# Performance work log

Hardware: AMD Instinct MI355X
Metric: run time of the kernel (lower is better)

The kernel has to match this reference:

```python
import jax, jax.numpy as jnp
import numpy as np

D_MODEL = 512
D_HEAD = 64
N_HEADS = D_MODEL // D_HEAD  # 8
KSIZE = 7


def setup_inputs() -> dict:
    key = jax.random.key(0)
    k1, k2, k3 = jax.random.split(key, 3)
    x = jax.random.normal(k1, (2, 48, 48, D_MODEL), dtype=jnp.float32)
    # torch Linear(d, 3d, bias=False): y = x @ W.T ; store transposed weight directly
    w_qkv = jax.random.normal(k2, (D_MODEL, 3 * D_MODEL), dtype=jnp.float32) * 0.02
    w_out = jax.random.normal(k3, (D_MODEL, D_MODEL), dtype=jnp.float32) * 0.02
    return {"x": x, "w_qkv": w_qkv, "w_out": w_out}


def _nbhd_idx(L, k):
    # NATTEN semantics: window centered at each pixel, shifted (clamped) to stay
    # fully inside the image near borders. Returns [L, k] absolute indices.
    start = jnp.clip(jnp.arange(L) - k // 2, 0, L - k)
    return start[:, None] + jnp.arange(k)[None, :]


def reference(x, w_qkv, w_out):
    n, h, w, _ = x.shape
    qkv = (x @ w_qkv).reshape(n, h, w, 3, N_HEADS, D_HEAD)
    qkv = jnp.transpose(qkv, (3, 0, 4, 1, 2, 5))  # [3, n, nh, h, w, e]
    q, k, v = qkv[0], qkv[1], qkv[2]
    q = q / jnp.asarray(D_HEAD, q.dtype) ** 0.5

    ih = _nbhd_idx(h, KSIZE)  # [h, k]
    iw = _nbhd_idx(w, KSIZE)  # [w, k]
    IH = ih[:, None, :, None]  # [h,1,k,1]
    IW = iw[None, :, None, :]  # [1,w,1,k]

    # gather per-pixel 2D neighborhoods: [n, nh, h, w, ka, kb, e]
    k_nb = k[:, :, IH, IW, :]
    logits = jnp.einsum('nghwe,nghwabe->nghwab', q, k_nb)
    logits = logits.reshape(n, N_HEADS, h, w, KSIZE * KSIZE)
    attn = jax.nn.softmax(logits, axis=-1).reshape(n, N_HEADS, h, w, KSIZE, KSIZE)

    v_nb = v[:, :, IH, IW, :]
    o = jnp.einsum('nghwab,nghwabe->nghwe', attn, v_nb)  # [n, nh, h, w, e]
    o = jnp.transpose(o, (0, 2, 3, 1, 4)).reshape(n, h, w, N_HEADS * D_HEAD)
    return o @ w_out
```

## Files before the change

kernel.cpp:

```cpp
#include <hip/hip_runtime.h>
#include <hip/hip_bf16.h>

typedef __bf16 bf16x4 __attribute__((ext_vector_type(4)));
typedef __bf16 bf16x8 __attribute__((ext_vector_type(8)));
typedef float f32x4 __attribute__((ext_vector_type(4)));

#define N_PIX 4608
#define D_MODEL 512
#define QKV_N 1536

__device__ __forceinline__ void gload_lds16(const void* g, void* l) {
  __builtin_amdgcn_global_load_lds(
      (const __attribute__((address_space(1))) unsigned int*)g,
      (__attribute__((address_space(3))) unsigned int*)l, 16, 0, 0);
}

__global__ __launch_bounds__(256) void prep_kernel(
    const float* __restrict__ x, const float* __restrict__ wq,
    const float* __restrict__ wo, __bf16* __restrict__ xbf,
    __bf16* __restrict__ wqT, __bf16* __restrict__ woT) {
  int b = blockIdx.x, tid = threadIdx.x;
  if (b < 2304) {
    int i = b * 1024 + tid * 4;
    float4 v = *(const float4*)&x[i];
    bf16x4 o = {(__bf16)v.x, (__bf16)v.y, (__bf16)v.z, (__bf16)v.w};
    *(bf16x4*)&xbf[i] = o;
    return;
  }
  __shared__ float tile[32][33];
  const float* src; __bf16* dst; int R, C, bx, by;
  bool is_wq;
  if (b < 3072) {
    int t = b - 2304; src = wq; dst = wqT; R = 512; C = 1536;
    bx = (t % 48) * 32; by = (t / 48) * 32; is_wq = true;
  } else {
    int t = b - 3072; src = wo; dst = woT; R = 512; C = 512;
    bx = (t & 15) * 32; by = (t >> 4) * 32; is_wq = false;
  }
  int tx = tid & 31, ty = tid >> 5;
#pragma unroll
  for (int i = 0; i < 32; i += 8)
    tile[ty + i][tx] = src[(by + ty + i) * C + bx + tx];
  __syncthreads();
#pragma unroll
  for (int i = 0; i < 32; i += 8) {
    int outrow = bx + ty + i;
    float v = tile[tx][ty + i];
    if (is_wq && outrow < 512) v *= 0.125f;
    dst[outrow * R + by + tx] = (__bf16)v;
  }
}

template <int BM, int BN>
__global__ __launch_bounds__(256) void gemm_kernel(
    const __bf16* __restrict__ A, const __bf16* __restrict__ Bt,
    void* __restrict__ C, int M, int N, int K, int c_is_f32) {
  constexpr int MT = BM / 32;
  constexpr int NT = BN / 32;
  constexpr int AR = BM / 4;
  constexpr int BR = BN / 4;
  __shared__ __bf16 sA[2][BM * 32];
  __shared__ __bf16 sB[2][BN * 32];
  int tid = threadIdx.x;
  int wv = tid >> 6, lane = tid & 63;
  int quad = lane >> 4, r16 = lane & 15;
  int m0 = blockIdx.y * BM, n0 = blockIdx.x * BN;

  int rA = lane >> 2;
  int kc = (lane & 3) * 8;
  const __bf16* Ag0 = A + (long)(m0 + wv * AR + rA) * K + kc;
  const __bf16* Bg0 = Bt + (long)(n0 + wv * BR + rA) * K + kc;

  int mw = (wv & 1) * (BM / 2), nw = (wv >> 1) * (BN / 2);

  f32x4 acc[MT][NT];
#pragma unroll
  for (int mt = 0; mt < MT; ++mt)
#pragma unroll
    for (int nt = 0; nt < NT; ++nt) acc[mt][nt] = f32x4{0.f, 0.f, 0.f, 0.f};

  auto stage = [&](int buf, int k0) {
    gload_lds16(Ag0 + k0, &sA[buf][(wv * AR) * 32]);
    if (AR == 32)
      gload_lds16(Ag0 + (long)16 * K + k0, &sA[buf][(wv * AR + 16) * 32]);
    gload_lds16(Bg0 + k0, &sB[buf][(wv * BR) * 32]);
    if (BR == 32)
      gload_lds16(Bg0 + (long)16 * K + k0, &sB[buf][(wv * BR + 16) * 32]);
  };

  stage(0, 0);
  int cur = 0;
  for (int k0 = 0; k0 < K; k0 += 32) {
    __syncthreads();
    if (k0 + 32 < K) stage(cur ^ 1, k0 + 32);
    bf16x8 af[MT], bfr[NT];
#pragma unroll
    for (int mt = 0; mt < MT; ++mt)
      af[mt] = *(const bf16x8*)&sA[cur][(mw + mt * 16 + r16) * 32 + quad * 8];
#pragma unroll
    for (int nt = 0; nt < NT; ++nt)
      bfr[nt] = *(const bf16x8*)&sB[cur][(nw + nt * 16 + r16) * 32 + quad * 8];
#pragma unroll
    for (int mt = 0; mt < MT; ++mt)
#pragma unroll
      for (int nt = 0; nt < NT; ++nt)
        acc[mt][nt] = __builtin_amdgcn_mfma_f32_16x16x32_bf16(af[mt], bfr[nt], acc[mt][nt], 0, 0, 0);
    cur ^= 1;
  }

  __bf16* Cb = (__bf16*)C;
  float* Cf = (float*)C;
#pragma unroll
  for (int mt = 0; mt < MT; ++mt)
#pragma unroll
    for (int r = 0; r < 4; ++r) {
      int row = m0 + mw + mt * 16 + quad * 4 + r;
#pragma unroll
      for (int nt = 0; nt < NT; ++nt) {
        int col = n0 + nw + nt * 16 + r16;
        float v = acc[mt][nt][r];
        if (c_is_f32) Cf[(long)row * N + col] = v;
        else          Cb[(long)row * N + col] = (__bf16)v;
      }
    }
}

#define KSTR 72
__global__ __launch_bounds__(512) void natten_attn_kernel(
    const __bf16* __restrict__ qkv, __bf16* __restrict__ o) {
  __shared__ __bf16 sK[196 * KSTR];
  __shared__ __bf16 sV[196 * KSTR];
  int tid = threadIdx.x;
  int bid = blockIdx.x;
  int nB = bid / 288;
  int rem = bid - nB * 288;
  int head = rem / 36;
  int tile = rem - head * 36;
  int tr = tile / 6, tc = tile - tr * 6;
  int r0 = tr * 8, c0 = tc * 8;
  int loH = r0 - 3; loH = loH < 0 ? 0 : (loH > 41 ? 41 : loH);
  int loW = c0 - 3; loW = loW < 0 ? 0 : (loW > 41 ? 41 : loW);

  for (int j = tid; j < 196 * 8; j += 512) {
    int rowi = j >> 3, ch = j & 7;
    int rr = rowi / 14, cc = rowi - rr * 14;
    int hh = loH + rr; hh = hh > 47 ? 47 : hh;
    int wp = loW + cc; wp = wp > 47 ? 47 : wp;
    long base = (long)(nB * 2304 + hh * 48 + wp) * QKV_N + head * 64 + ch * 8;
    *(uint4*)&sK[rowi * KSTR + ch * 8] = *(const uint4*)&qkv[base + 512];
    *(uint4*)&sV[rowi * KSTR + ch * 8] = *(const uint4*)&qkv[base + 1024];
  }
  __syncthreads();

  int q = tid >> 3, s = tid & 7;
  int qr = q >> 3, qc = q & 7;
  int h = r0 + qr, w = c0 + qc;
  int pix = nB * 2304 + h * 48 + w;
  int hs = h - 3; hs = hs < 0 ? 0 : (hs > 41 ? 41 : hs); hs -= loH;
  int ws = w - 3; ws = ws < 0 ? 0 : (ws > 41 ? 41 : ws); ws -= loW;
  int base = (hs * 14 + ws) * KSTR + s * 8;

  bf16x8 q0 = *(const bf16x8*)&qkv[(long)pix * QKV_N + head * 64 + s * 8];
  float qf[8];
#pragma unroll
  for (int t = 0; t < 8; ++t) qf[t] = (float)q0[t];

  float lg[49];
#pragma unroll
  for (int j = 0; j < 49; ++j) {
    int a = j / 7, b = j % 7;
    bf16x8 k0 = *(const bf16x8*)&sK[base + (a * 14 + b) * KSTR];
    float acc = 0.f;
#pragma unroll
    for (int t = 0; t < 8; ++t) acc = fmaf(qf[t], (float)k0[t], acc);
    acc += __shfl_xor(acc, 1);
    acc += __shfl_xor(acc, 2);
    acc += __shfl_xor(acc, 4);
    lg[j] = acc;
  }

  float mx = lg[0];
#pragma unroll
  for (int j = 1; j < 49; ++j) mx = fmaxf(mx, lg[j]);
  float sm = 0.f;
#pragma unroll
  for (int j = 0; j < 49; ++j) { lg[j] = __expf(lg[j] - mx); sm += lg[j]; }
  float inv = 1.f / sm;

  float ov[8];
#pragma unroll
  for (int t = 0; t < 8; ++t) ov[t] = 0.f;
#pragma unroll
  for (int j = 0; j < 49; ++j) {
    int a = j / 7, b = j % 7;
    float pj = lg[j] * inv;
    bf16x8 v0 = *(const bf16x8*)&sV[base + (a * 14 + b) * KSTR];
#pragma unroll
    for (int t = 0; t < 8; ++t) ov[t] = fmaf(pj, (float)v0[t], ov[t]);
  }

  bf16x8 o0;
#pragma unroll
  for (int t = 0; t < 8; ++t) o0[t] = (__bf16)ov[t];
  *(bf16x8*)&o[(long)pix * D_MODEL + head * 64 + s * 8] = o0;
}


extern "C" void kernel_launch(void* const* d_in, const int* in_sizes, int n_in,
                              void* d_out, int out_size, void* d_ws, size_t ws_size,
                              hipStream_t stream) {
  const float* x = (const float*)d_in[0];
  const float* w_qkv = (const float*)d_in[1];
  const float* w_out = (const float*)d_in[2];
  float* out = (float*)d_out;

  __bf16* ws = (__bf16*)d_ws;
  __bf16* xbf   = ws;
  __bf16* wqkvT = xbf + N_PIX * D_MODEL;
  __bf16* woutT = wqkvT + QKV_N * D_MODEL;
  __bf16* qkvb  = woutT + D_MODEL * D_MODEL;
  __bf16* obf   = qkvb + N_PIX * QKV_N;

  prep_kernel<<<3328, 256, 0, stream>>>(x, w_qkv, w_out, xbf, wqkvT, woutT);
  gemm_kernel<128, 128><<<dim3(QKV_N / 128, N_PIX / 128), 256, 0, stream>>>(
      xbf, wqkvT, qkvb, N_PIX, QKV_N, D_MODEL, 0);
  natten_attn_kernel<<<576, 512, 0, stream>>>(qkvb, obf);
  gemm_kernel<64, 128><<<dim3(D_MODEL / 128, N_PIX / 64), 256, 0, stream>>>(
      obf, woutT, out, N_PIX, D_MODEL, D_MODEL, 1);
}
```

Measured before the change: 121.9 us.

## Compute neighborhood attention with MFMA over dense 8x8 query tile vs 14x14 halo

Replaces per-thread scalar dot products in the neighborhood attention kernel with MFMA matrix ops. Each 64-query tile computes logits against all 196 halo keys, masks positions outside each query's 7x7 window, softmaxes in registers, writes probabilities to LDS, and does a second MFMA against a transposed V. K and Q are staged via direct global-to-LDS loads with an XOR swizzle. This does about 4x redundant FLOPs (196 vs 49 keys) but moves the work from VALU to matrix cores, and it adds a scalar transpose store for V.

After: 115.2 us. 1.06x faster.

```diff
diff --git a/kernel.cpp b/kernel.cpp
--- a/kernel.cpp
+++ b/kernel.cpp
@@ -125,12 +125,18 @@
     }
 }
 
-#define KSTR 72
-__global__ __launch_bounds__(512) void natten_attn_kernel(
+__global__ __launch_bounds__(256) void natten_attn_kernel(
     const __bf16* __restrict__ qkv, __bf16* __restrict__ o) {
-  __shared__ __bf16 sK[196 * KSTR];
-  __shared__ __bf16 sV[196 * KSTR];
+  __shared__ __bf16 sKP[16384];
+  __shared__ __bf16 sVT[16384];
+  __shared__ __bf16 sQ[4096];
+  char* kB = (char*)sKP;
+  char* vB = (char*)sVT;
+  char* qB = (char*)sQ;
+
   int tid = threadIdx.x;
+  int lane = tid & 63, wv = tid >> 6;
+  int quad = lane >> 4, r16 = lane & 15;
   int bid = blockIdx.x;
   int nB = bid / 288;
   int rem = bid - nB * 288;
@@ -140,69 +146,148 @@
   int r0 = tr * 8, c0 = tc * 8;
   int loH = r0 - 3; loH = loH < 0 ? 0 : (loH > 41 ? 41 : loH);
   int loW = c0 - 3; loW = loW < 0 ? 0 : (loW > 41 ? 41 : loW);
-
-  for (int j = tid; j < 196 * 8; j += 512) {
-    int rowi = j >> 3, ch = j & 7;
-    int rr = rowi / 14, cc = rowi - rr * 14;
-    int hh = loH + rr; hh = hh > 47 ? 47 : hh;
-    int wp = loW + cc; wp = wp > 47 ? 47 : wp;
-    long base = (long)(nB * 2304 + hh * 48 + wp) * QKV_N + head * 64 + ch * 8;
-    *(uint4*)&sK[rowi * KSTR + ch * 8] = *(const uint4*)&qkv[base + 512];
-    *(uint4*)&sV[rowi * KSTR + ch * 8] = *(const uint4*)&qkv[base + 1024];
+  long hb = (long)head * 64;
+
+  {
+    int rl = lane >> 3, cc = lane & 7;
+#pragma unroll
+    for (int it = 0; it < 7; ++it) {
+      int g = wv * 7 + it;
+      int row = g * 8 + rl;
+      int pos = row > 195 ? 195 : row;
+      int pr = pos / 14, pc = pos - pr * 14;
+      int hh = loH + pr; hh = hh > 47 ? 47 : hh;
+      int wp = loW + pc; wp = wp > 47 ? 47 : wp;
+      int csrc = cc ^ (row & 7);
+      const __bf16* src = qkv + (long)(nB * 2304 + hh * 48 + wp) * QKV_N + 512 + hb + csrc * 8;
+      gload_lds16(src, kB + g * 1024);
+    }
+#pragma unroll
+    for (int it = 0; it < 2; ++it) {
+      int g = wv * 2 + it;
+      int row = g * 8 + rl;
+      int csrc = cc ^ (row & 7);
+      int pix = nB * 2304 + (r0 + (row >> 3)) * 48 + c0 + (row & 7);
+      const __bf16* src = qkv + (long)pix * QKV_N + hb + csrc * 8;
+      gload_lds16(src, qB + g * 1024);
+    }
+  }
+#pragma unroll
+  for (int it = 0; it < 7; ++it) {
+    int idx = tid + it * 256;
+    int pos = idx >> 3, cb = idx & 7;
+    int pp = pos > 195 ? 195 : pos;
+    int pr = pp / 14, pc = pp - pr * 14;
+    int hh = loH + pr; hh = hh > 47 ? 47 : hh;
+    int wp = loW + pc; wp = wp > 47 ? 47 : wp;
+    bf16x8 v = *(const bf16x8*)(qkv + (long)(nB * 2304 + hh * 48 + wp) * QKV_N + 1024 + hb + cb * 8);
+#pragma unroll
+    for (int i = 0; i < 8; ++i) {
+      int ch = cb * 8 + i;
+      *(__bf16*)(vB + ch * 512 + ((2 * pos) ^ ((ch & 7) << 4))) = v[i];
+    }
   }
   __syncthreads();
 
-  int q = tid >> 3, s = tid & 7;
-  int qr = q >> 3, qc = q & 7;
-  int h = r0 + qr, w = c0 + qc;
-  int pix = nB * 2304 + h * 48 + w;
-  int hs = h - 3; hs = hs < 0 ? 0 : (hs > 41 ? 41 : hs); hs -= loH;
-  int ws = w - 3; ws = ws < 0 ? 0 : (ws > 41 ? 41 : ws); ws -= loW;
-  int base = (hs * 14 + ws) * KSTR + s * 8;
-
-  bf16x8 q0 = *(const bf16x8*)&qkv[(long)pix * QKV_N + head * 64 + s * 8];
-  float qf[8];
-#pragma unroll
-  for (int t = 0; t < 8; ++t) qf[t] = (float)q0[t];
-
-  float lg[49];
-#pragma unroll
-  for (int j = 0; j < 49; ++j) {
-    int a = j / 7, b = j % 7;
-    bf16x8 k0 = *(const bf16x8*)&sK[base + (a * 14 + b) * KSTR];
-    float acc = 0.f;
-#pragma unroll
-    for (int t = 0; t < 8; ++t) acc = fmaf(qf[t], (float)k0[t], acc);
-    acc += __shfl_xor(acc, 1);
-    acc += __shfl_xor(acc, 2);
-    acc += __shfl_xor(acc, 4);
-    lg[j] = acc;
-  }
-
-  float mx = lg[0];
-#pragma unroll
-  for (int j = 1; j < 49; ++j) mx = fmaxf(mx, lg[j]);
-  float sm = 0.f;
-#pragma unroll
-  for (int j = 0; j < 49; ++j) { lg[j] = __expf(lg[j] - mx); sm += lg[j]; }
-  float inv = 1.f / sm;
-
-  float ov[8];
-#pragma unroll
-  for (int t = 0; t < 8; ++t) ov[t] = 0.f;
-#pragma unroll
-  for (int j = 0; j < 49; ++j) {
-    int a = j / 7, b = j % 7;
-    float pj = lg[j] * inv;
-    bf16x8 v0 = *(const bf16x8*)&sV[base + (a * 14 + b) * KSTR];
-#pragma unroll
-    for (int t = 0; t < 8; ++t) ov[t] = fmaf(pj, (float)v0[t], ov[t]);
-  }
-
-  bf16x8 o0;
-#pragma unroll
-  for (int t = 0; t < 8; ++t) o0[t] = (__bf16)ov[t];
-  *(bf16x8*)&o[(long)pix * D_MODEL + head * 64 + s * 8] = o0;
+  int rowq = wv * 16 + r16;
+  int swq = (rowq & 7) << 4;
+  bf16x8 aq0 = *(const bf16x8*)(qB + rowq * 128 + ((quad * 16) ^ swq));
+  bf16x8 aq1 = *(const bf16x8*)(qB + rowq * 128 + ((64 + quad * 16) ^ swq));
+  f32x4 acc[14];
+#pragma unroll
+  for (int nt = 0; nt < 14; ++nt) acc[nt] = f32x4{0.f, 0.f, 0.f, 0.f};
+#pragma unroll
+  for (int nt = 0; nt < 14; ++nt) {
+    int rk = nt * 16 + r16;
+    int swk = (rk & 7) << 4;
+    bf16x8 b0 = *(const bf16x8*)(kB + rk * 128 + ((quad * 16) ^ swk));
+    bf16x8 b1 = *(const bf16x8*)(kB + rk * 128 + ((64 + quad * 16) ^ swk));
+    acc[nt] = __builtin_amdgcn_mfma_f32_16x16x32_bf16(aq0, b0, acc[nt], 0, 0, 0);
+    acc[nt] = __builtin_amdgcn_mfma_f32_16x16x32_bf16(aq1, b1, acc[nt], 0, 0, 0);
+  }
+
+  int hs[4], wsX[4];
+#pragma unroll
+  for (int r = 0; r < 4; ++r) {
+    int q = wv * 16 + quad * 4 + r;
+    int h = r0 + (q >> 3), w = c0 + (q & 7);
+    int a = h - 3; a = a < 0 ? 0 : (a > 41 ? 41 : a);
+    int b = w - 3; b = b < 0 ? 0 : (b > 41 ? 41 : b);
+    hs[r] = a - loH; wsX[r] = b - loW;
+  }
+  {
+    int pr = r16 >= 14 ? 1 : 0;
+    int pc = r16 - pr * 14;
+#pragma unroll
+    for (int nt = 0; nt < 14; ++nt) {
+      bool pv = (nt * 16 + r16) < 196;
+#pragma unroll
+      for (int r = 0; r < 4; ++r) {
+        bool ok = pv && (unsigned)(pr - hs[r]) <= 6u && (unsigned)(pc - wsX[r]) <= 6u;
+        acc[nt][r] = ok ? acc[nt][r] : -1e30f;
+      }
+      pc += 2; pr += 1;
+      if (pc >= 14) { pc -= 14; pr += 1; }
+    }
+  }
+  float inv[4];
+#pragma unroll
+  for (int r = 0; r < 4; ++r) {
+    float m = acc[0][r];
+#pragma unroll
+    for (int nt = 1; nt < 14; ++nt) m = fmaxf(m, acc[nt][r]);
+    m = fmaxf(m, __shfl_xor(m, 1));
+    m = fmaxf(m, __shfl_xor(m, 2));
+    m = fmaxf(m, __shfl_xor(m, 4));
+    m = fmaxf(m, __shfl_xor(m, 8));
+    float s = 0.f;
+#pragma unroll
+    for (int nt = 0; nt < 14; ++nt) { float e = __expf(acc[nt][r] - m); acc[nt][r] = e; s += e; }
+    s += __shfl_xor(s, 1);
+    s += __shfl_xor(s, 2);
+    s += __shfl_xor(s, 4);
+    s += __shfl_xor(s, 8);
+    inv[r] = 1.f / s;
+  }
+  __syncthreads();
+
+#pragma unroll
+  for (int r = 0; r < 4; ++r) {
+    int q = wv * 16 + quad * 4 + r;
+    char* rowp = kB + q * 512;
+    int sw = (q & 7) << 4;
+#pragma unroll
+    for (int nt = 0; nt < 14; ++nt) {
+      int pos = nt * 16 + r16;
+      *(__bf16*)(rowp + ((2 * pos) ^ sw)) = (__bf16)acc[nt][r];
+    }
+  }
+  __syncthreads();
+
+  f32x4 acc2[4];
+#pragma unroll
+  for (int nt = 0; nt < 4; ++nt) acc2[nt] = f32x4{0.f, 0.f, 0.f, 0.f};
+#pragma unroll
+  for (int ks = 0; ks < 7; ++ks) {
+    bf16x8 ap = *(const bf16x8*)(kB + rowq * 512 + ((ks * 64 + quad * 16) ^ swq));
+#pragma unroll
+    for (int nt = 0; nt < 4; ++nt) {
+      int rc = nt * 16 + r16;
+      bf16x8 bv = *(const bf16x8*)(vB + rc * 512 + ((ks * 64 + quad * 16) ^ ((rc & 7) << 4)));
+      acc2[nt] = __builtin_amdgcn_mfma_f32_16x16x32_bf16(ap, bv, acc2[nt], 0, 0, 0);
+    }
+  }
+
+#pragma unroll
+  for (int r = 0; r < 4; ++r) {
+    int q = wv * 16 + quad * 4 + r;
+    long pix = nB * 2304 + (long)(r0 + (q >> 3)) * 48 + c0 + (q & 7);
+    __bf16* op = o + pix * D_MODEL + hb;
+    float iv = inv[r];
+#pragma unroll
+    for (int nt = 0; nt < 4; ++nt)
+      op[nt * 16 + r16] = (__bf16)(acc2[nt][r] * iv);
+  }
 }
 
 
@@ -224,7 +309,7 @@
   prep_kernel<<<3328, 256, 0, stream>>>(x, w_qkv, w_out, xbf, wqkvT, woutT);
   gemm_kernel<128, 128><<<dim3(QKV_N / 128, N_PIX / 128), 256, 0, stream>>>(
       xbf, wqkvT, qkvb, N_PIX, QKV_N, D_MODEL, 0);
-  natten_attn_kernel<<<576, 512, 0, stream>>>(qkvb, obf);
+  natten_attn_kernel<<<576, 256, 0, stream>>>(qkvb, obf);
   gemm_kernel<64, 128><<<dim3(D_MODEL / 128, N_PIX / 64), 256, 0, stream>>>(
       obf, woutT, out, N_PIX, D_MODEL, D_MODEL, 1);
 }
```
